# Kernel tuning notes

Hardware: AMD Instinct MI355X
Metric: run time of the kernel (lower is better)

Reference implementation:

```python
import jax, jax.numpy as jnp
import numpy as np


def setup_inputs() -> dict:
    key = jax.random.key(0)
    k1, k2, k3 = jax.random.split(key, 3)
    B, S, E = 4, 8192, 1024
    x = jax.random.normal(k1, (B, S, E), dtype=jnp.float32)
    # torch nn.Linear weights have shape [out_features, in_features]
    W1 = jax.random.normal(k2, (3 * E, E), dtype=jnp.float32) * (1.0 / np.sqrt(E))
    W2 = jax.random.normal(k3, (E, E), dtype=jnp.float32) * (1.0 / np.sqrt(E))
    return {"x": x, "W1": W1, "W2": W2, "heads": 16}


def reference(x, W1, W2, heads):
    B, S, E = x.shape
    h = heads
    e = E // h
    # qkv projection: [B,S,3E] -> 'b s (n h e) -> n b h s e'
    qkv = (x @ W1.T).reshape(B, S, 3, h, e)
    qkv = jnp.transpose(qkv, (2, 0, 3, 1, 4))  # [3,B,h,S,e]
    q, k, v = qkv[0], qkv[1], qkv[2]
    # score: [B,h,e,e], softmax over last dim (c)
    score = jax.nn.softmax(jnp.einsum('bhnk,bhnc->bhkc', k / 4, v), axis=-1)
    # einsum 'bhnk,bhkc->bhnk': elementwise over k, sum over c
    attn = jax.nn.softmax(jnp.einsum('bhnk,bhkc->bhnk', q / 4, score), axis=-1)
    # 'b h s e -> b s (h e)' then linear_2
    out = jnp.transpose(attn, (0, 2, 1, 3)).reshape(B, S, E) @ W2.T
    return out
```

## Files before the change

kernel.cpp:

```cpp
#include <hip/hip_runtime.h>
#include <hip/hip_bf16.h>
#include <stdint.h>

static constexpr int MTOT = 32768;
static constexpr int KD   = 1024;
static constexpr int ND   = 1024;

static constexpr int BM = 256, BN = 256, BK = 64;
static constexpr int NT = KD / BK;
static constexpr int BUF_BYTES = 65536;
static constexpr int BOFF = 32768;
static constexpr int HALF = 16384;

typedef __bf16 bf16x8 __attribute__((ext_vector_type(8)));
typedef float  f32x4  __attribute__((ext_vector_type(4)));

__device__ __forceinline__ unsigned short f2bf_rne(float f) {
  union { float f; uint32_t u; } c; c.f = f;
  uint32_t u = c.u;
  return (unsigned short)((u + 0x7fffu + ((u >> 16) & 1u)) >> 16);
}

__global__ void cast_f32_to_bf16(const float* __restrict__ src,
                                 unsigned short* __restrict__ dst, int n4) {
  int idx = blockIdx.x * blockDim.x + threadIdx.x;
  int stride = gridDim.x * blockDim.x;
  for (int i = idx; i < n4; i += stride) {
    float4 v = reinterpret_cast<const float4*>(src)[i];
    ushort4 o;
    o.x = f2bf_rne(v.x); o.y = f2bf_rne(v.y);
    o.z = f2bf_rne(v.z); o.w = f2bf_rne(v.w);
    reinterpret_cast<ushort4*>(dst)[i] = o;
  }
}

__device__ __forceinline__ void gload_lds16(const void* g, void* lds) {
  __builtin_amdgcn_global_load_lds(
      (const __attribute__((address_space(1))) unsigned int*)g,
      (__attribute__((address_space(3))) unsigned int*)lds, 16, 0, 0);
}

template <int SOFTMAX>
__global__ __launch_bounds__(512, 2)
void gemm8(const unsigned short* __restrict__ A,
           const unsigned short* __restrict__ Bm,
           void* __restrict__ Cout) {
  extern __shared__ __align__(16) char ldsc[];

  const int tid  = threadIdx.x;
  const int lane = tid & 63;
  const int wid  = tid >> 6;
  const int wm = wid >> 2, wn = wid & 3;
  const int fr = lane & 15, fq = lane >> 4;

  const int bid0 = blockIdx.x;
  const int bid  = ((bid0 & 7) << 6) | (bid0 >> 3);
  const int brow = (bid >> 2) * BM;
  const int bcol = (bid & 3) * BN;

  const int srow  = tid >> 3;
  const int sslot = (tid & 7) ^ (srow & 7);
  const unsigned short* gA = A  + (size_t)(brow + srow) * KD + sslot * 8;
  const unsigned short* gB = Bm + (size_t)(bcol + srow) * KD + sslot * 8;
  const int wofs = tid * 16;

  f32x4  acc[8][4] = {};
  bf16x8 a0[4][2], a1[4][2], bA[2][2], bB[2][2];

  auto STAGE = [&](const unsigned short* g, int h, int kt, int b, int opOff) {
    const unsigned short* gu = g + (size_t)(h * 128) * KD + kt * BK;
    char* du = ldsc + b * BUF_BYTES + opOff + h * HALF + (wid << 10);
    gload_lds16(gu, du);
    gload_lds16(gu + (size_t)64 * KD, du + 8192);
  };

  auto rdA = [&](int b, bf16x8 (*dst)[2], int mBase) {
    const char* base = ldsc + b * BUF_BYTES + wm * HALF;
    #pragma unroll
    for (int mm = 0; mm < 4; ++mm) {
      const int r = (mBase + mm) * 16 + fr;
      #pragma unroll
      for (int ks = 0; ks < 2; ++ks)
        dst[mm][ks] = *(const bf16x8*)(base + (r << 7) +
                        ((ks * 64 + fq * 16) ^ ((r & 7) << 4)));
    }
  };
  auto rdB = [&](int b, int nBase, bf16x8 (*dst)[2]) {
    const char* base = ldsc + b * BUF_BYTES + BOFF + (wn >> 1) * HALF;
    #pragma unroll
    for (int nn = 0; nn < 2; ++nn) {
      const int r = (wn & 1) * 64 + (nBase + nn) * 16 + fr;
      #pragma unroll
      for (int ks = 0; ks < 2; ++ks)
        dst[nn][ks] = *(const bf16x8*)(base + (r << 7) +
                       ((ks * 64 + fq * 16) ^ ((r & 7) << 4)));
    }
  };
  auto MFMA16 = [&](int mBase, int nBase, bf16x8 (*af)[2], bf16x8 (*bf)[2]) {
    #pragma unroll
    for (int mm = 0; mm < 4; ++mm)
      #pragma unroll
      for (int nn = 0; nn < 2; ++nn)
        #pragma unroll
        for (int ks = 0; ks < 2; ++ks)
          acc[mBase + mm][nBase + nn] = __builtin_amdgcn_mfma_f32_16x16x32_bf16(
              af[mm][ks], bf[nn][ks], acc[mBase + mm][nBase + nn], 0, 0, 0);
  };

  STAGE(gA, 0, 0, 0, 0);    STAGE(gA, 1, 0, 0, 0);
  STAGE(gB, 0, 0, 0, BOFF); STAGE(gB, 1, 0, 0, BOFF);
  STAGE(gA, 0, 1, 1, 0);    STAGE(gA, 1, 1, 1, 0);
  asm volatile("s_waitcnt vmcnt(4)" ::: "memory");
  __builtin_amdgcn_s_barrier();
  rdB(0, 0, bA);

  for (int T = 0; T < NT; ++T) {
    const int cur = T & 1, nxt = cur ^ 1;
    const int tp1 = (T + 1 < NT) ? T + 1 : NT - 1;
    const int tp2 = (T + 2 < NT) ? T + 2 : NT - 1;

    rdA(cur, a0, 0);
    STAGE(gB, 0, tp1, nxt, BOFF);
    __builtin_amdgcn_s_barrier();
    asm volatile("s_waitcnt lgkmcnt(0)" ::: "memory");
    __builtin_amdgcn_s_setprio(1);
    MFMA16(0, 0, a0, bA);
    __builtin_amdgcn_s_setprio(0);
    __builtin_amdgcn_s_barrier();

    rdA(cur, a1, 4);
    STAGE(gB, 1, tp1, nxt, BOFF);
    __builtin_amdgcn_s_barrier();
    asm volatile("s_waitcnt lgkmcnt(0)" ::: "memory");
    __builtin_amdgcn_s_setprio(1);
    MFMA16(4, 0, a1, bA);
    __builtin_amdgcn_s_setprio(0);
    __builtin_amdgcn_s_barrier();

    rdB(cur, 2, bB);
    STAGE(gA, 0, tp2, cur, 0);
    __builtin_amdgcn_s_barrier();
    asm volatile("s_waitcnt lgkmcnt(0)" ::: "memory");
    __builtin_amdgcn_s_setprio(1);
    MFMA16(4, 2, a1, bB);
    __builtin_amdgcn_s_setprio(0);
    __builtin_amdgcn_s_barrier();

    STAGE(gA, 1, tp2, cur, 0);
    asm volatile("s_waitcnt vmcnt(4)" ::: "memory");
    __builtin_amdgcn_s_barrier();
    rdB(nxt, 0, bA);
    __builtin_amdgcn_s_setprio(1);
    MFMA16(0, 2, a0, bB);
    __builtin_amdgcn_s_setprio(0);
    __builtin_amdgcn_s_barrier();
  }

  if constexpr (SOFTMAX) {
    unsigned short* attn = reinterpret_cast<unsigned short*>(Cout);
    constexpr float CEXP = 0.25f * 1.44269504088896340736f;
    #pragma unroll
    for (int m = 0; m < 8; ++m) {
      const int row = brow + wm * 128 + m * 16 + fq * 4;
      #pragma unroll
      for (int j = 0; j < 4; ++j) {
        float v0 = acc[m][0][j], v1 = acc[m][1][j];
        float v2 = acc[m][2][j], v3 = acc[m][3][j];
        float mx = fmaxf(fmaxf(v0, v1), fmaxf(v2, v3));
        #pragma unroll
        for (int s = 1; s < 16; s <<= 1) mx = fmaxf(mx, __shfl_xor(mx, s, 64));
        float p0 = exp2f((v0 - mx) * CEXP);
        float p1 = exp2f((v1 - mx) * CEXP);
        float p2 = exp2f((v2 - mx) * CEXP);
        float p3 = exp2f((v3 - mx) * CEXP);
        float sm = p0 + p1 + p2 + p3;
        #pragma unroll
        for (int s = 1; s < 16; s <<= 1) sm += __shfl_xor(sm, s, 64);
        const float inv = 1.0f / sm;
        unsigned short* dst =
            attn + (size_t)(row + j) * ND + (bcol + wn * 64 + fr);
        dst[0]  = f2bf_rne(p0 * inv);
        dst[16] = f2bf_rne(p1 * inv);
        dst[32] = f2bf_rne(p2 * inv);
        dst[48] = f2bf_rne(p3 * inv);
      }
    }
  } else {
    float* Cf = reinterpret_cast<float*>(Cout);
    #pragma unroll
    for (int m = 0; m < 8; ++m) {
      const int row = brow + wm * 128 + m * 16 + fq * 4;
      #pragma unroll
      for (int n = 0; n < 4; ++n) {
        const int col = bcol + wn * 64 + n * 16 + fr;
        #pragma unroll
        for (int j = 0; j < 4; ++j)
          Cf[(size_t)(row + j) * ND + col] = acc[m][n][j];
      }
    }
  }
}

extern "C" void kernel_launch(void* const* d_in, const int* in_sizes, int n_in,
                              void* d_out, int out_size, void* d_ws, size_t ws_size,
                              hipStream_t stream) {
  const float* x  = (const float*)d_in[0];
  const float* W1 = (const float*)d_in[1];
  const float* W2 = (const float*)d_in[2];
  float* out = (float*)d_out;

  char* ws = (char*)d_ws;
  unsigned short* xb   = (unsigned short*)(ws);
  unsigned short* w1b  = (unsigned short*)(ws + (size_t)67108864);
  unsigned short* w2b  = (unsigned short*)(ws + (size_t)69206016);
  unsigned short* attn = (unsigned short*)(ws + (size_t)71303168);

  hipFuncSetAttribute(reinterpret_cast<const void*>(gemm8<1>),
                      hipFuncAttributeMaxDynamicSharedMemorySize, 131072);
  hipFuncSetAttribute(reinterpret_cast<const void*>(gemm8<0>),
                      hipFuncAttributeMaxDynamicSharedMemorySize, 131072);

  cast_f32_to_bf16<<<2048, 256, 0, stream>>>(x,  xb,  MTOT * KD / 4);
  cast_f32_to_bf16<<<512,  256, 0, stream>>>(W1, w1b, KD * KD / 4);
  cast_f32_to_bf16<<<512,  256, 0, stream>>>(W2, w2b, KD * KD / 4);

  const int nblk = (MTOT / BM) * (ND / BN);
  gemm8<1><<<nblk, 512, 131072, stream>>>(xb, w1b, (void*)attn);
  gemm8<0><<<nblk, 512, 131072, stream>>>(attn, w2b, (void*)out);
}
```

Before: 197.5 us.

## Switch GEMM to 32x32x16 bf16 MFMA tiles and drop pre-MFMA barriers

Replaces the 16x16x32 MFMA micro-tiling with 32x32x16 bf16 MFMA. Fragment loads, LDS swizzle addressing and accumulator layout change to match, and the softmax and store epilogues are rewritten for the 32-lane output layout. The larger instruction is meant to cut LDS fragment reads and instruction count per FLOP. The barrier between each stage issue and its MFMA block is also removed to reduce synchronization stalls. The barrier removal carries some ordering risk.

```diff
diff --git a/kernel.cpp b/kernel.cpp
--- a/kernel.cpp
+++ b/kernel.cpp
@@ -13,7 +13,7 @@
 static constexpr int HALF = 16384;
 
 typedef __bf16 bf16x8 __attribute__((ext_vector_type(8)));
-typedef float  f32x4  __attribute__((ext_vector_type(4)));
+typedef float  f32x16 __attribute__((ext_vector_type(16)));
 
 __device__ __forceinline__ unsigned short f2bf_rne(float f) {
   union { float f; uint32_t u; } c; c.f = f;
@@ -51,7 +51,9 @@
   const int lane = tid & 63;
   const int wid  = tid >> 6;
   const int wm = wid >> 2, wn = wid & 3;
-  const int fr = lane & 15, fq = lane >> 4;
+  const int l31 = lane & 31;
+  const int hi  = lane >> 5;
+  const int swz = (lane & 7) << 4;
 
   const int bid0 = blockIdx.x;
   const int bid  = ((bid0 & 7) << 6) | (bid0 >> 3);
@@ -62,10 +64,9 @@
   const int sslot = (tid & 7) ^ (srow & 7);
   const unsigned short* gA = A  + (size_t)(brow + srow) * KD + sslot * 8;
   const unsigned short* gB = Bm + (size_t)(bcol + srow) * KD + sslot * 8;
-  const int wofs = tid * 16;
-
-  f32x4  acc[8][4] = {};
-  bf16x8 a0[4][2], a1[4][2], bA[2][2], bB[2][2];
+
+  f32x16 acc[4][2] = {};
+  bf16x8 a0[2][4], a1[2][4], bA[4], bB[4];
 
   auto STAGE = [&](const unsigned short* g, int h, int kt, int b, int opOff) {
     const unsigned short* gu = g + (size_t)(h * 128) * KD + kt * BK;
@@ -74,37 +75,32 @@
     gload_lds16(gu + (size_t)64 * KD, du + 8192);
   };
 
-  auto rdA = [&](int b, bf16x8 (*dst)[2], int mBase) {
+  auto rdA = [&](int b, bf16x8 (*dst)[4], int mgBase) {
     const char* base = ldsc + b * BUF_BYTES + wm * HALF;
     #pragma unroll
-    for (int mm = 0; mm < 4; ++mm) {
-      const int r = (mBase + mm) * 16 + fr;
-      #pragma unroll
-      for (int ks = 0; ks < 2; ++ks)
-        dst[mm][ks] = *(const bf16x8*)(base + (r << 7) +
-                        ((ks * 64 + fq * 16) ^ ((r & 7) << 4)));
+    for (int i = 0; i < 2; ++i) {
+      const int r = (mgBase + i) * 32 + l31;
+      #pragma unroll
+      for (int ks = 0; ks < 4; ++ks)
+        dst[i][ks] = *(const bf16x8*)(base + (r << 7) +
+                       ((ks * 32 + hi * 16) ^ swz));
     }
   };
-  auto rdB = [&](int b, int nBase, bf16x8 (*dst)[2]) {
+  auto rdB = [&](int b, bf16x8* dst, int ng) {
     const char* base = ldsc + b * BUF_BYTES + BOFF + (wn >> 1) * HALF;
-    #pragma unroll
-    for (int nn = 0; nn < 2; ++nn) {
-      const int r = (wn & 1) * 64 + (nBase + nn) * 16 + fr;
-      #pragma unroll
-      for (int ks = 0; ks < 2; ++ks)
-        dst[nn][ks] = *(const bf16x8*)(base + (r << 7) +
-                       ((ks * 64 + fq * 16) ^ ((r & 7) << 4)));
-    }
-  };
-  auto MFMA16 = [&](int mBase, int nBase, bf16x8 (*af)[2], bf16x8 (*bf)[2]) {
-    #pragma unroll
-    for (int mm = 0; mm < 4; ++mm)
-      #pragma unroll
-      for (int nn = 0; nn < 2; ++nn)
-        #pragma unroll
-        for (int ks = 0; ks < 2; ++ks)
-          acc[mBase + mm][nBase + nn] = __builtin_amdgcn_mfma_f32_16x16x32_bf16(
-              af[mm][ks], bf[nn][ks], acc[mBase + mm][nBase + nn], 0, 0, 0);
+    const int r = (wn & 1) * 64 + ng * 32 + l31;
+    #pragma unroll
+    for (int ks = 0; ks < 4; ++ks)
+      dst[ks] = *(const bf16x8*)(base + (r << 7) +
+                   ((ks * 32 + hi * 16) ^ swz));
+  };
+  auto MFMA8 = [&](int mgBase, int ng, bf16x8 (*af)[4], bf16x8* bf) {
+    #pragma unroll
+    for (int ks = 0; ks < 4; ++ks)
+      #pragma unroll
+      for (int i = 0; i < 2; ++i)
+        acc[mgBase + i][ng] = __builtin_amdgcn_mfma_f32_32x32x16_bf16(
+            af[i][ks], bf[ks], acc[mgBase + i][ng], 0, 0, 0);
   };
 
   STAGE(gA, 0, 0, 0, 0);    STAGE(gA, 1, 0, 0, 0);
@@ -112,7 +108,7 @@
   STAGE(gA, 0, 1, 1, 0);    STAGE(gA, 1, 1, 1, 0);
   asm volatile("s_waitcnt vmcnt(4)" ::: "memory");
   __builtin_amdgcn_s_barrier();
-  rdB(0, 0, bA);
+  rdB(0, bA, 0);
 
   for (int T = 0; T < NT; ++T) {
     const int cur = T & 1, nxt = cur ^ 1;
@@ -121,37 +117,34 @@
 
     rdA(cur, a0, 0);
     STAGE(gB, 0, tp1, nxt, BOFF);
-    __builtin_amdgcn_s_barrier();
     asm volatile("s_waitcnt lgkmcnt(0)" ::: "memory");
     __builtin_amdgcn_s_setprio(1);
-    MFMA16(0, 0, a0, bA);
-    __builtin_amdgcn_s_setprio(0);
-    __builtin_amdgcn_s_barrier();
-
-    rdA(cur, a1, 4);
+    MFMA8(0, 0, a0, bA);
+    __builtin_amdgcn_s_setprio(0);
+    __builtin_amdgcn_s_barrier();
+
+    rdA(cur, a1, 2);
     STAGE(gB, 1, tp1, nxt, BOFF);
-    __builtin_amdgcn_s_barrier();
     asm volatile("s_waitcnt lgkmcnt(0)" ::: "memory");
     __builtin_amdgcn_s_setprio(1);
-    MFMA16(4, 0, a1, bA);
-    __builtin_amdgcn_s_setprio(0);
-    __builtin_amdgcn_s_barrier();
-
-    rdB(cur, 2, bB);
+    MFMA8(2, 0, a1, bA);
+    __builtin_amdgcn_s_setprio(0);
+    __builtin_amdgcn_s_barrier();
+
+    rdB(cur, bB, 1);
     STAGE(gA, 0, tp2, cur, 0);
-    __builtin_amdgcn_s_barrier();
     asm volatile("s_waitcnt lgkmcnt(0)" ::: "memory");
     __builtin_amdgcn_s_setprio(1);
-    MFMA16(4, 2, a1, bB);
+    MFMA8(2, 1, a1, bB);
     __builtin_amdgcn_s_setprio(0);
     __builtin_amdgcn_s_barrier();
 
     STAGE(gA, 1, tp2, cur, 0);
     asm volatile("s_waitcnt vmcnt(4)" ::: "memory");
     __builtin_amdgcn_s_barrier();
-    rdB(nxt, 0, bA);
-    __builtin_amdgcn_s_setprio(1);
-    MFMA16(0, 2, a0, bB);
+    rdB(nxt, bA, 0);
+    __builtin_amdgcn_s_setprio(1);
+    MFMA8(0, 1, a0, bB);
     __builtin_amdgcn_s_setprio(0);
     __builtin_amdgcn_s_barrier();
   }
@@ -160,42 +153,39 @@
     unsigned short* attn = reinterpret_cast<unsigned short*>(Cout);
     constexpr float CEXP = 0.25f * 1.44269504088896340736f;
     #pragma unroll
-    for (int m = 0; m < 8; ++m) {
-      const int row = brow + wm * 128 + m * 16 + fq * 4;
-      #pragma unroll
-      for (int j = 0; j < 4; ++j) {
-        float v0 = acc[m][0][j], v1 = acc[m][1][j];
-        float v2 = acc[m][2][j], v3 = acc[m][3][j];
-        float mx = fmaxf(fmaxf(v0, v1), fmaxf(v2, v3));
+    for (int mg = 0; mg < 4; ++mg) {
+      #pragma unroll
+      for (int reg = 0; reg < 16; ++reg) {
+        const int row = brow + wm * 128 + mg * 32 +
+                        (reg & 3) + 8 * (reg >> 2) + 4 * hi;
+        float v0 = acc[mg][0][reg], v1 = acc[mg][1][reg];
+        float mx = fmaxf(v0, v1);
         #pragma unroll
-        for (int s = 1; s < 16; s <<= 1) mx = fmaxf(mx, __shfl_xor(mx, s, 64));
+        for (int s = 1; s < 32; s <<= 1) mx = fmaxf(mx, __shfl_xor(mx, s, 64));
         float p0 = exp2f((v0 - mx) * CEXP);
         float p1 = exp2f((v1 - mx) * CEXP);
-        float p2 = exp2f((v2 - mx) * CEXP);
-        float p3 = exp2f((v3 - mx) * CEXP);
-        float sm = p0 + p1 + p2 + p3;
+        float sm = p0 + p1;
         #pragma unroll
-        for (int s = 1; s < 16; s <<= 1) sm += __shfl_xor(sm, s, 64);
+        for (int s = 1; s < 32; s <<= 1) sm += __shfl_xor(sm, s, 64);
         const float inv = 1.0f / sm;
-        unsigned short* dst =
-            attn + (size_t)(row + j) * ND + (bcol + wn * 64 + fr);
+        unsigned short* dst = attn + (size_t)row * ND + (bcol + wn * 64 + l31);
         dst[0]  = f2bf_rne(p0 * inv);
-        dst[16] = f2bf_rne(p1 * inv);
-        dst[32] = f2bf_rne(p2 * inv);
-        dst[48] = f2bf_rne(p3 * inv);
+        dst[32] = f2bf_rne(p1 * inv);
       }
     }
   } else {
     float* Cf = reinterpret_cast<float*>(Cout);
     #pragma unroll
-    for (int m = 0; m < 8; ++m) {
-      const int row = brow + wm * 128 + m * 16 + fq * 4;
-      #pragma unroll
-      for (int n = 0; n < 4; ++n) {
-        const int col = bcol + wn * 64 + n * 16 + fr;
+    for (int mg = 0; mg < 4; ++mg) {
+      #pragma unroll
+      for (int ng = 0; ng < 2; ++ng) {
         #pragma unroll
-        for (int j = 0; j < 4; ++j)
-          Cf[(size_t)(row + j) * ND + col] = acc[m][n][j];
+        for (int reg = 0; reg < 16; ++reg) {
+          const int row = brow + wm * 128 + mg * 32 +
+                          (reg & 3) + 8 * (reg >> 2) + 4 * hi;
+          Cf[(size_t)row * ND + (bcol + wn * 64 + ng * 32 + l31)] =
+              acc[mg][ng][reg];
+        }
       }
     }
   }
```

New measurement: 228.0 us. +15.5%, slower.

## Fuse fp32-to-bf16 cast of x into the first GEMM's A-tile loading

Applied to the files above, without the earlier changes.

Removes the standalone kernel that cast x to bf16. The first GEMM now loads fp32 x tiles into registers, converts them to bf16 and writes them into the same swizzled LDS layout, interleaved with the existing pipeline through adjusted vmcnt waits. This avoids writing a bf16 copy of x and reading it back. The cost is reading fp32 x, twice the bytes, once per column block, plus extra registers and VALU conversion work inside the main loop.

```diff
diff --git a/kernel.cpp b/kernel.cpp
--- a/kernel.cpp
+++ b/kernel.cpp
@@ -40,9 +40,9 @@
       (__attribute__((address_space(3))) unsigned int*)lds, 16, 0, 0);
 }
 
-template <int SOFTMAX>
+template <int SOFTMAX, int AF32>
 __global__ __launch_bounds__(512, 2)
-void gemm8(const unsigned short* __restrict__ A,
+void gemm8(const void* __restrict__ Asrc,
            const unsigned short* __restrict__ Bm,
            void* __restrict__ Cout) {
   extern __shared__ __align__(16) char ldsc[];
@@ -60,12 +60,14 @@
 
   const int srow  = tid >> 3;
   const int sslot = (tid & 7) ^ (srow & 7);
-  const unsigned short* gA = A  + (size_t)(brow + srow) * KD + sslot * 8;
+  const unsigned short* gA =
+      (const unsigned short*)Asrc + (size_t)(brow + srow) * KD + sslot * 8;
+  const float* gXf = (const float*)Asrc + (size_t)(brow + srow) * KD + sslot * 8;
   const unsigned short* gB = Bm + (size_t)(bcol + srow) * KD + sslot * 8;
-  const int wofs = tid * 16;
 
   f32x4  acc[8][4] = {};
   bf16x8 a0[4][2], a1[4][2], bA[2][2], bB[2][2];
+  float4 av[4][2];
 
   auto STAGE = [&](const unsigned short* g, int h, int kt, int b, int opOff) {
     const unsigned short* gu = g + (size_t)(h * 128) * KD + kt * BK;
@@ -73,6 +75,28 @@
     gload_lds16(gu, du);
     gload_lds16(gu + (size_t)64 * KD, du + 8192);
   };
+  auto A_ISSUE = [&](int kt, int uLo, int uHi) {
+    #pragma unroll
+    for (int u = 0; u < 4; ++u)
+      if (u >= uLo && u < uHi) {
+        const float* gp = gXf + (size_t)(u * 64) * KD + kt * BK;
+        av[u][0] = *reinterpret_cast<const float4*>(gp);
+        av[u][1] = *reinterpret_cast<const float4*>(gp + 4);
+      }
+  };
+  auto A_WRITE = [&](int b) {
+    #pragma unroll
+    for (int u = 0; u < 4; ++u) {
+      bf16x8 w;
+      #pragma unroll
+      for (int j = 0; j < 4; ++j) {
+        w[j]     = (__bf16)av[u][0][j];
+        w[j + 4] = (__bf16)av[u][1][j];
+      }
+      *reinterpret_cast<bf16x8*>(
+          ldsc + b * BUF_BYTES + (u >> 1) * HALF + (u & 1) * 8192 + tid * 16) = w;
+    }
+  };
 
   auto rdA = [&](int b, bf16x8 (*dst)[2], int mBase) {
     const char* base = ldsc + b * BUF_BYTES + wm * HALF;
@@ -107,10 +131,20 @@
               af[mm][ks], bf[nn][ks], acc[mBase + mm][nBase + nn], 0, 0, 0);
   };
 
-  STAGE(gA, 0, 0, 0, 0);    STAGE(gA, 1, 0, 0, 0);
-  STAGE(gB, 0, 0, 0, BOFF); STAGE(gB, 1, 0, 0, BOFF);
-  STAGE(gA, 0, 1, 1, 0);    STAGE(gA, 1, 1, 1, 0);
-  asm volatile("s_waitcnt vmcnt(4)" ::: "memory");
+  if constexpr (AF32) {
+    A_ISSUE(0, 0, 4);
+    asm volatile("s_waitcnt vmcnt(0)" ::: "memory");
+    A_WRITE(0);
+    STAGE(gB, 0, 0, 0, BOFF); STAGE(gB, 1, 0, 0, BOFF);
+    A_ISSUE(1, 0, 4);
+    asm volatile("s_waitcnt vmcnt(8)" ::: "memory");
+    asm volatile("s_waitcnt lgkmcnt(0)" ::: "memory");
+  } else {
+    STAGE(gA, 0, 0, 0, 0);    STAGE(gA, 1, 0, 0, 0);
+    STAGE(gB, 0, 0, 0, BOFF); STAGE(gB, 1, 0, 0, BOFF);
+    STAGE(gA, 0, 1, 1, 0);    STAGE(gA, 1, 1, 1, 0);
+    asm volatile("s_waitcnt vmcnt(4)" ::: "memory");
+  }
   __builtin_amdgcn_s_barrier();
   rdB(0, 0, bA);
 
@@ -121,6 +155,10 @@
 
     rdA(cur, a0, 0);
     STAGE(gB, 0, tp1, nxt, BOFF);
+    if constexpr (AF32) {
+      asm volatile("s_waitcnt vmcnt(2)" ::: "memory");
+      A_WRITE(nxt);
+    }
     __builtin_amdgcn_s_barrier();
     asm volatile("s_waitcnt lgkmcnt(0)" ::: "memory");
     __builtin_amdgcn_s_setprio(1);
@@ -138,7 +176,8 @@
     __builtin_amdgcn_s_barrier();
 
     rdB(cur, 2, bB);
-    STAGE(gA, 0, tp2, cur, 0);
+    if constexpr (AF32) A_ISSUE(tp2, 0, 2);
+    else                STAGE(gA, 0, tp2, cur, 0);
     __builtin_amdgcn_s_barrier();
     asm volatile("s_waitcnt lgkmcnt(0)" ::: "memory");
     __builtin_amdgcn_s_setprio(1);
@@ -146,8 +185,13 @@
     __builtin_amdgcn_s_setprio(0);
     __builtin_amdgcn_s_barrier();
 
-    STAGE(gA, 1, tp2, cur, 0);
-    asm volatile("s_waitcnt vmcnt(4)" ::: "memory");
+    if constexpr (AF32) {
+      A_ISSUE(tp2, 2, 4);
+      asm volatile("s_waitcnt vmcnt(8)" ::: "memory");
+    } else {
+      STAGE(gA, 1, tp2, cur, 0);
+      asm volatile("s_waitcnt vmcnt(4)" ::: "memory");
+    }
     __builtin_amdgcn_s_barrier();
     rdB(nxt, 0, bA);
     __builtin_amdgcn_s_setprio(1);
@@ -210,21 +254,19 @@
   float* out = (float*)d_out;
 
   char* ws = (char*)d_ws;
-  unsigned short* xb   = (unsigned short*)(ws);
   unsigned short* w1b  = (unsigned short*)(ws + (size_t)67108864);
   unsigned short* w2b  = (unsigned short*)(ws + (size_t)69206016);
   unsigned short* attn = (unsigned short*)(ws + (size_t)71303168);
 
-  hipFuncSetAttribute(reinterpret_cast<const void*>(gemm8<1>),
+  hipFuncSetAttribute(reinterpret_cast<const void*>(gemm8<1, 1>),
                       hipFuncAttributeMaxDynamicSharedMemorySize, 131072);
-  hipFuncSetAttribute(reinterpret_cast<const void*>(gemm8<0>),
+  hipFuncSetAttribute(reinterpret_cast<const void*>(gemm8<0, 0>),
                       hipFuncAttributeMaxDynamicSharedMemorySize, 131072);
 
-  cast_f32_to_bf16<<<2048, 256, 0, stream>>>(x,  xb,  MTOT * KD / 4);
-  cast_f32_to_bf16<<<512,  256, 0, stream>>>(W1, w1b, KD * KD / 4);
-  cast_f32_to_bf16<<<512,  256, 0, stream>>>(W2, w2b, KD * KD / 4);
+  cast_f32_to_bf16<<<512, 256, 0, stream>>>(W1, w1b, KD * KD / 4);
+  cast_f32_to_bf16<<<512, 256, 0, stream>>>(W2, w2b, KD * KD / 4);
 
   const int nblk = (MTOT / BM) * (ND / BN);
-  gemm8<1><<<nblk, 512, 131072, stream>>>(xb, w1b, (void*)attn);
-  gemm8<0><<<nblk, 512, 131072, stream>>>(attn, w2b, (void*)out);
-}
+  gemm8<1, 1><<<nblk, 512, 131072, stream>>>((const void*)x, w1b, (void*)attn);
+  gemm8<0, 0><<<nblk, 512, 131072, stream>>>((const void*)attn, w2b, (void*)out);
+}
```

After: 268.5 us. 1.36x slower.
